# Kernel optimization log

Measured on AMD Instinct MI355X. Metric: run time of the kernel, lower is better.

The kernel has to match this reference:

```python
import jax, jax.numpy as jnp
import numpy as np

D_MODEL = 1024
H = 16
D_K = D_MODEL // H
NEG = -1e9


def setup_inputs() -> dict:
    key = jax.random.key(0)
    ks = jax.random.split(key, 13)
    B, S = 4, 2048
    q = jax.random.normal(ks[0], (B, S, D_MODEL), dtype=jnp.float32)
    k = jax.random.normal(ks[1], (B, S, D_MODEL), dtype=jnp.float32)
    v = jax.random.normal(ks[2], (B, S, D_MODEL), dtype=jnp.float32)
    mask = jax.random.randint(ks[3], (B, 1, S, S), 0, 2, dtype=jnp.int32)
    s = 1.0 / np.sqrt(D_MODEL)
    wq = jax.random.uniform(ks[4], (D_MODEL, D_MODEL), jnp.float32, -s, s)
    bq = jax.random.uniform(ks[5], (D_MODEL,), jnp.float32, -s, s)
    wk = jax.random.uniform(ks[6], (D_MODEL, D_MODEL), jnp.float32, -s, s)
    bk = jax.random.uniform(ks[7], (D_MODEL,), jnp.float32, -s, s)
    wv = jax.random.uniform(ks[8], (D_MODEL, D_MODEL), jnp.float32, -s, s)
    bv = jax.random.uniform(ks[9], (D_MODEL,), jnp.float32, -s, s)
    wo = jax.random.uniform(ks[10], (D_MODEL, D_MODEL), jnp.float32, -s, s)
    bo = jax.random.uniform(ks[11], (D_MODEL,), jnp.float32, -s, s)
    return {"q": q, "k": k, "v": v, "mask": mask,
            "wq": wq, "bq": bq, "wk": wk, "bk": bk,
            "wv": wv, "bv": bv, "wo": wo, "bo": bo}


def reference(q, k, v, mask, wq, bq, wk, bk, wv, bv, wo, bo):
    B, S, _ = q.shape
    # projections (torch Linear: x @ W.T + b)
    query = q @ wq.T + bq
    key_ = k @ wk.T + bk
    value = v @ wv.T + bv
    # [B, S, H, D_K] -> [B, H, S, D_K]
    query = query.reshape(B, S, H, D_K).transpose(0, 2, 1, 3)
    key_ = key_.reshape(B, S, H, D_K).transpose(0, 2, 1, 3)
    value = value.reshape(B, S, H, D_K).transpose(0, 2, 1, 3)
    scores = jnp.einsum('bhqd,bhkd->bhqk', query, key_) / jnp.sqrt(jnp.float32(D_K))
    scores = jnp.where(mask == 0, jnp.float32(NEG), scores)
    attn = jax.nn.softmax(scores, axis=-1)  # dropout p=0 -> identity
    x = jnp.einsum('bhqk,bhkd->bhqd', attn, value)
    x = x.transpose(0, 2, 1, 3).reshape(B, S, D_MODEL)
    return x @ wo.T + bo
```

## Files before the change

### kernel.cpp

```cpp
#include <hip/hip_runtime.h>
#include <stdint.h>
#include <stddef.h>


typedef unsigned short ushort_t;
typedef unsigned long long u64;
typedef __attribute__((ext_vector_type(8))) short short8;
typedef __attribute__((ext_vector_type(4))) float floatx4;
typedef __attribute__((ext_vector_type(4))) unsigned short ushort4v;
typedef __attribute__((ext_vector_type(4))) unsigned int uint4v;

#define QSCALE (0.125f * 1.4426950408889634f)

__device__ __forceinline__ ushort_t f2bf(float f) {
    union { float ff; unsigned int i; } v; v.ff = f;
    unsigned int u = v.i;
    return (ushort_t)((u + 0x7fffu + ((u >> 16) & 1u)) >> 16);
}
__device__ __forceinline__ unsigned int pack2bf(float a, float b) {
    union { float f; unsigned int i; } ua, ub; ua.f = a; ub.f = b;
    return ((ua.i + 0x8000u) >> 16) | ((ub.i + 0x8000u) & 0xffff0000u);
}
__device__ __forceinline__ float fexp2(float x) {
#if __has_builtin(__builtin_amdgcn_exp2f)
    return __builtin_amdgcn_exp2f(x);
#else
    return exp2f(x);
#endif
}
__device__ __forceinline__ void g2l16(const void* g, void* l) {
    __builtin_amdgcn_global_load_lds(
        (const __attribute__((address_space(1))) void*)(uintptr_t)g,
        (__attribute__((address_space(3))) void*)(uint32_t)(uintptr_t)l,
        16, 0, 0);
}

__global__ __launch_bounds__(256) void conv_w4(
    const float* __restrict__ w0, const float* __restrict__ w1,
    const float* __restrict__ w2, const float* __restrict__ w3,
    ushort_t* __restrict__ out)
{
    const int seg = blockIdx.y;
    const float* src = (seg == 0) ? w0 : (seg == 1) ? w1 : (seg == 2) ? w2 : w3;
    const int i = blockIdx.x * 256 + threadIdx.x;
    const float4 v = ((const float4*)src)[i];
    ushort4v o;
    o.x = f2bf(v.x); o.y = f2bf(v.y); o.z = f2bf(v.z); o.w = f2bf(v.w);
    ((ushort4v*)(out + (size_t)seg * 1024 * 1024))[i] = o;
}

__global__ __launch_bounds__(256) void mask_pack(
    const int* __restrict__ m, u64* __restrict__ out)
{
    const int gid = blockIdx.x * 256 + threadIdx.x;
    const u64 bits = __ballot(m[gid] != 0);
    if ((threadIdx.x & 63) == 0) out[gid >> 6] = bits;
}

template <int MODE, int AF32>
__global__ __launch_bounds__(256, 2) void gemm_bt(
    const void* __restrict__ Ain, const ushort_t* __restrict__ W,
    const float* __restrict__ bias, void* __restrict__ Cout, float scale)
{
    constexpr int N = 1024, K = 1024;
    __shared__ alignas(16) ushort_t As[128 * 32];
    __shared__ alignas(16) ushort_t Bs[128 * 32];

    const int tid  = threadIdx.x;
    const int lane = tid & 63;
    const int w    = tid >> 6;
    const int quad = lane >> 4;
    const int l16  = lane & 15;
    const int wm = w >> 1, wn = w & 1;
    const int bm = blockIdx.x * 128, bn = blockIdx.y * 128;

    const int ar0 = tid >> 2,         acs0 = ((tid & 3) ^ (ar0 & 3)) * 8;
    const int ar1 = (tid + 256) >> 2, acs1 = ((tid & 3) ^ (ar1 & 3)) * 8;

    const ushort_t* Wst0 = W + (size_t)(bn + ar0) * K + acs0;
    const ushort_t* Wst1 = W + (size_t)(bn + ar1) * K + acs1;

    const int arow = tid >> 1, ahalf = tid & 1;
    const float* Af = (const float*)Ain + (size_t)(bm + arow) * K + ahalf * 16;
    const int ac0 = ((2 * ahalf + 0) ^ (arow & 3)) * 8;
    const int ac1 = ((2 * ahalf + 1) ^ (arow & 3)) * 8;

    const ushort_t* Ast0 = (const ushort_t*)Ain + (size_t)(bm + ar0) * K + acs0;
    const ushort_t* Ast1 = (const ushort_t*)Ain + (size_t)(bm + ar1) * K + acs1;

    const int ksw = (quad ^ (l16 & 3)) * 8;
    int asoff[4], bsoff[4];
#pragma unroll
    for (int i = 0; i < 4; i++) {
        asoff[i] = (wm * 64 + i * 16 + l16) * 32 + ksw;
        bsoff[i] = (wn * 64 + i * 16 + l16) * 32 + ksw;
    }

    floatx4 acc[4][4] = {};

    for (int kt = 0; kt < K; kt += 32) {
        float4 f0, f1, f2, f3;
        if (AF32) {
            const float4* ap = (const float4*)(Af + kt);
            f0 = ap[0]; f1 = ap[1]; f2 = ap[2]; f3 = ap[3];
        }
        __syncthreads();
        if (AF32) {
            uint4v c0, c1;
            c0.x = pack2bf(f0.x, f0.y); c0.y = pack2bf(f0.z, f0.w);
            c0.z = pack2bf(f1.x, f1.y); c0.w = pack2bf(f1.z, f1.w);
            c1.x = pack2bf(f2.x, f2.y); c1.y = pack2bf(f2.z, f2.w);
            c1.z = pack2bf(f3.x, f3.y); c1.w = pack2bf(f3.z, f3.w);
            *(uint4v*)&As[arow * 32 + ac0] = c0;
            *(uint4v*)&As[arow * 32 + ac1] = c1;
        } else {
            g2l16(Ast0 + kt, &As[tid * 8]);
            g2l16(Ast1 + kt, &As[(tid + 256) * 8]);
        }
        g2l16(Wst0 + kt, &Bs[tid * 8]);
        g2l16(Wst1 + kt, &Bs[(tid + 256) * 8]);
        __syncthreads();

        short8 af[4], bf[4];
#pragma unroll
        for (int i = 0; i < 4; i++) af[i] = *(const short8*)&As[asoff[i]];
#pragma unroll
        for (int i = 0; i < 4; i++) bf[i] = *(const short8*)&Bs[bsoff[i]];
#pragma unroll
        for (int mi = 0; mi < 4; mi++)
#pragma unroll
            for (int ni = 0; ni < 4; ni++)
                acc[mi][ni] = __builtin_amdgcn_mfma_f32_16x16x32_bf16(
                    af[mi], bf[ni], acc[mi][ni], 0, 0, 0);
    }

#pragma unroll
    for (int ni = 0; ni < 4; ni++) {
        const int n = bn + wn * 64 + ni * 16 + l16;
        const float bv = bias[n];
#pragma unroll
        for (int mi = 0; mi < 4; mi++) {
            const int mbase = bm + wm * 64 + mi * 16 + quad * 4;
            if (MODE == 2) {
                const int b_ = mbase >> 11, s0 = mbase & 2047;
                const int h = n >> 6, d = n & 63;
                ushort4v pk;
#pragma unroll
                for (int r = 0; r < 4; r++)
                    pk[r] = f2bf((acc[mi][ni][r] + bv) * scale);
                *(ushort4v*)&((ushort_t*)Cout)[
                    (((size_t)(b_ * 16 + h)) * 64 + d) * 2048 + s0] = pk;
            } else {
#pragma unroll
                for (int r = 0; r < 4; r++) {
                    const int m = mbase + r;
                    const float of = (acc[mi][ni][r] + bv) * scale;
                    if (MODE == 0) {
                        ((float*)Cout)[(size_t)m * N + n] = of;
                    } else {
                        const int b_ = m >> 11, s = m & 2047;
                        const int h = n >> 6, d = n & 63;
                        ((ushort_t*)Cout)[(((size_t)(b_ * 16 + h)) * 2048 + s) * 64 + d]
                            = f2bf(of);
                    }
                }
            }
        }
    }
}

__global__ __launch_bounds__(256, 3) void attn(
    const ushort_t* __restrict__ Q,
    const ushort_t* __restrict__ Kk,
    const ushort_t* __restrict__ Vt,
    const u64* __restrict__ mb,
    ushort_t* __restrict__ X)
{
    constexpr int S = 2048;
    __shared__ alignas(16) ushort_t Ks[64 * 64];
    __shared__ alignas(16) ushort_t Vs[64 * 64];
    __shared__ alignas(16) ushort_t Ps[4][16 * 64];

    const int tid  = threadIdx.x;
    const int lane = tid & 63;
    const int w    = tid >> 6;
    const int quad = lane >> 4;
    const int l16  = lane & 15;
    const int bh = blockIdx.x;
    const int b  = bh >> 4, h = bh & 15;
    const int qbase = blockIdx.y * 64 + w * 16;
    const int qlane = qbase + l16;

    const int r0 = tid >> 3,         cs0 = ((tid & 7) ^ (r0 & 7)) * 8;
    const int r1 = (tid + 256) >> 3, cs1 = ((tid & 7) ^ (r1 & 7)) * 8;

    const ushort_t* Kst0 = &Kk[((size_t)bh * S + r0) * 64 + cs0];
    const ushort_t* Kst1 = &Kk[((size_t)bh * S + r1) * 64 + cs1];
    const ushort_t* Vst0 = &Vt[((size_t)bh * 64 + r0) * S + cs0];
    const ushort_t* Vst1 = &Vt[((size_t)bh * 64 + r1) * S + cs1];

    const int swz = l16 & 7;
    int kvoff[2][4], pfoff[2], pwoff[4];
#pragma unroll
    for (int ks = 0; ks < 2; ks++) {
        pfoff[ks] = l16 * 64 + (((ks * 4 + quad) ^ swz) * 8);
#pragma unroll
        for (int ni = 0; ni < 4; ni++)
            kvoff[ks][ni] = (ni * 16 + l16) * 64 + (((ks * 4 + quad) ^ swz) * 8);
    }
#pragma unroll
    for (int ni = 0; ni < 4; ni++)
        pwoff[ni] = l16 * 64 + (((ni * 2 + (quad >> 1)) ^ swz) * 8) + (quad & 1) * 4;
    ushort_t* Psw = &Ps[w][0];

    short8 qf[2];
#pragma unroll
    for (int ks = 0; ks < 2; ks++)
        qf[ks] = *(const short8*)&Q[((size_t)bh * S + qlane) * 64 + ks * 32 + quad * 8];

    short8 onesv;
#pragma unroll
    for (int i = 0; i < 8; i++) onesv[i] = (short)0x3F80;

    const u64* mrow = mb + ((size_t)b * S + qlane) * 32;

    floatx4 o[4] = {};
    floatx4 lf = {};

    for (int kt = 0; kt < 32; kt++) {
        __syncthreads();
        g2l16(Kst0 + kt * 4096, &Ks[tid * 8]);
        g2l16(Kst1 + kt * 4096, &Ks[(tid + 256) * 8]);
        g2l16(Vst0 + kt * 64,   &Vs[tid * 8]);
        g2l16(Vst1 + kt * 64,   &Vs[(tid + 256) * 8]);
        __syncthreads();

        floatx4 s[4] = {};
#pragma unroll
        for (int ks = 0; ks < 2; ks++)
#pragma unroll
            for (int ni = 0; ni < 4; ni++)
                s[ni] = __builtin_amdgcn_mfma_f32_16x16x32_bf16(
                    *(const short8*)&Ks[kvoff[ks][ni]], qf[ks], s[ni], 0, 0, 0);

        const u64 mw = mrow[kt];
#pragma unroll
        for (int ni = 0; ni < 4; ni++) {
            const unsigned int t = (unsigned int)(mw >> (ni * 16 + quad * 4));
#pragma unroll
            for (int r = 0; r < 4; r++)
                s[ni][r] = (t & (1u << r)) ? fexp2(s[ni][r]) : 0.f;
        }

#pragma unroll
        for (int ni = 0; ni < 4; ni++) {
            unsigned int lo = pack2bf(s[ni][0], s[ni][1]);
            unsigned int hi = pack2bf(s[ni][2], s[ni][3]);
            unsigned long long dv = ((unsigned long long)hi << 32) | lo;
            *(unsigned long long*)&Psw[pwoff[ni]] = dv;
        }

#pragma unroll
        for (int ks = 0; ks < 2; ks++) {
            const short8 pf = *(const short8*)&Psw[pfoff[ks]];
            lf = __builtin_amdgcn_mfma_f32_16x16x32_bf16(onesv, pf, lf, 0, 0, 0);
#pragma unroll
            for (int ni = 0; ni < 4; ni++)
                o[ni] = __builtin_amdgcn_mfma_f32_16x16x32_bf16(
                    *(const short8*)&Vs[kvoff[ks][ni]], pf, o[ni], 0, 0, 0);
        }
    }

    const float inv = 1.0f / lf[0];
#pragma unroll
    for (int ni = 0; ni < 4; ni++) {
        ushort4v pk;
#pragma unroll
        for (int r = 0; r < 4; r++) pk[r] = f2bf(o[ni][r] * inv);
        *(ushort4v*)&X[((size_t)b * S + qlane) * 1024 + h * 64 + ni * 16 + quad * 4] = pk;
    }
}

extern "C" void kernel_launch(void* const* d_in, const int* in_sizes, int n_in,
                              void* d_out, int out_size, void* d_ws, size_t ws_size,
                              hipStream_t stream) {
    const float* q    = (const float*)d_in[0];
    const float* k    = (const float*)d_in[1];
    const float* v    = (const float*)d_in[2];
    const int*   mask = (const int*)d_in[3];
    const float* wq   = (const float*)d_in[4];
    const float* bq   = (const float*)d_in[5];
    const float* wk   = (const float*)d_in[6];
    const float* bk   = (const float*)d_in[7];
    const float* wv   = (const float*)d_in[8];
    const float* bv   = (const float*)d_in[9];
    const float* wo   = (const float*)d_in[10];
    const float* bo   = (const float*)d_in[11];

    const size_t MB = 1024 * 1024;
    uint8_t* ws = (uint8_t*)d_ws;
    ushort_t* Wb   = (ushort_t*)(ws);
    u64*      mbits= (u64*)(ws + 8 * MB);
    ushort_t* Qp   = (ushort_t*)(ws + 10 * MB);
    ushort_t* Kp   = (ushort_t*)(ws + 26 * MB);
    ushort_t* Vtp  = (ushort_t*)(ws + 42 * MB);
    ushort_t* Xp   = (ushort_t*)(ws + 58 * MB);

    dim3 blk(256);
    dim3 gg(64, 8);
    const int gW = (1024 * 1024) / 1024;
    const int gM = (4 * 2048 * 2048) / 256;

    conv_w4<<<dim3(gW, 4), blk, 0, stream>>>(wq, wk, wv, wo, Wb);
    mask_pack<<<gM, blk, 0, stream>>>(mask, mbits);

    gemm_bt<1, 1><<<gg, blk, 0, stream>>>(q, Wb,                bq, Qp,  QSCALE);
    gemm_bt<1, 1><<<gg, blk, 0, stream>>>(k, Wb + 1 * MB,       bk, Kp,  1.0f);
    gemm_bt<2, 1><<<gg, blk, 0, stream>>>(v, Wb + 2 * MB,       bv, Vtp, 1.0f);

    attn<<<dim3(64, 32), blk, 0, stream>>>(Qp, Kp, Vtp, mbits, Xp);

    gemm_bt<0, 0><<<gg, blk, 0, stream>>>(Xp, Wb + 3 * MB,      bo, d_out, 1.0f);
}
```

Before: 475.0 us.

## Batch QKV GEMMs into one launch, prefetch A, and double attention key tile

Merges the three QKV projection launches into a single gemm_qkv kernel indexed by blockIdx.z, and swaps the grid axes so consecutive blocks share the same activation rows. The fp32 A tile is now loaded one iteration ahead to hide global latency behind the MFMA work, and occupancy is raised to 3 blocks. The attention kernel processes 128 keys per iteration instead of 64, halving barrier and loop overhead at the cost of double the LDS per block, which may lower occupancy. The output GEMM becomes a separate specialised bf16 kernel.

New measurement: 483.0 us. About the same (+1.7%).

```diff
diff --git a/kernel.cpp b/kernel.cpp
--- a/kernel.cpp
+++ b/kernel.cpp
@@ -57,14 +57,23 @@
     if ((threadIdx.x & 63) == 0) out[gid >> 6] = bits;
 }
 
-template <int MODE, int AF32>
-__global__ __launch_bounds__(256, 2) void gemm_bt(
-    const void* __restrict__ Ain, const ushort_t* __restrict__ W,
-    const float* __restrict__ bias, void* __restrict__ Cout, float scale)
+__global__ __launch_bounds__(256, 3) void gemm_qkv(
+    const float* __restrict__ qin, const float* __restrict__ kin,
+    const float* __restrict__ vin, const ushort_t* __restrict__ Wall,
+    const float* __restrict__ bqp, const float* __restrict__ bkp,
+    const float* __restrict__ bvp, ushort_t* __restrict__ Qp,
+    ushort_t* __restrict__ Kp, ushort_t* __restrict__ Vtp)
 {
-    constexpr int N = 1024, K = 1024;
+    constexpr int K = 1024;
     __shared__ alignas(16) ushort_t As[128 * 32];
     __shared__ alignas(16) ushort_t Bs[128 * 32];
+
+    const int z = blockIdx.z;
+    const float* Ain = (z == 0) ? qin : (z == 1) ? kin : vin;
+    const ushort_t* W = Wall + (size_t)z * 1024 * 1024;
+    const float* bias = (z == 0) ? bqp : (z == 1) ? bkp : bvp;
+    const float scale = (z == 0) ? QSCALE : 1.0f;
+    ushort_t* Cout = (z == 0) ? Qp : (z == 1) ? Kp : Vtp;
 
     const int tid  = threadIdx.x;
     const int lane = tid & 63;
@@ -72,21 +81,17 @@
     const int quad = lane >> 4;
     const int l16  = lane & 15;
     const int wm = w >> 1, wn = w & 1;
-    const int bm = blockIdx.x * 128, bn = blockIdx.y * 128;
+    const int bm = blockIdx.y * 128, bn = blockIdx.x * 128;
 
     const int ar0 = tid >> 2,         acs0 = ((tid & 3) ^ (ar0 & 3)) * 8;
     const int ar1 = (tid + 256) >> 2, acs1 = ((tid & 3) ^ (ar1 & 3)) * 8;
-
     const ushort_t* Wst0 = W + (size_t)(bn + ar0) * K + acs0;
     const ushort_t* Wst1 = W + (size_t)(bn + ar1) * K + acs1;
 
     const int arow = tid >> 1, ahalf = tid & 1;
-    const float* Af = (const float*)Ain + (size_t)(bm + arow) * K + ahalf * 16;
+    const float* Af = Ain + (size_t)(bm + arow) * K + ahalf * 16;
     const int ac0 = ((2 * ahalf + 0) ^ (arow & 3)) * 8;
     const int ac1 = ((2 * ahalf + 1) ^ (arow & 3)) * 8;
-
-    const ushort_t* Ast0 = (const ushort_t*)Ain + (size_t)(bm + ar0) * K + acs0;
-    const ushort_t* Ast1 = (const ushort_t*)Ain + (size_t)(bm + ar1) * K + acs1;
 
     const int ksw = (quad ^ (l16 & 3)) * 8;
     int asoff[4], bsoff[4];
@@ -98,28 +103,31 @@
 
     floatx4 acc[4][4] = {};
 
+    float4 fA0, fA1, fA2, fA3;
+    {
+        const float4* ap = (const float4*)Af;
+        fA0 = ap[0]; fA1 = ap[1]; fA2 = ap[2]; fA3 = ap[3];
+    }
+
     for (int kt = 0; kt < K; kt += 32) {
-        float4 f0, f1, f2, f3;
-        if (AF32) {
-            const float4* ap = (const float4*)(Af + kt);
-            f0 = ap[0]; f1 = ap[1]; f2 = ap[2]; f3 = ap[3];
-        }
-        __syncthreads();
-        if (AF32) {
+        __syncthreads();
+        {
             uint4v c0, c1;
-            c0.x = pack2bf(f0.x, f0.y); c0.y = pack2bf(f0.z, f0.w);
-            c0.z = pack2bf(f1.x, f1.y); c0.w = pack2bf(f1.z, f1.w);
-            c1.x = pack2bf(f2.x, f2.y); c1.y = pack2bf(f2.z, f2.w);
-            c1.z = pack2bf(f3.x, f3.y); c1.w = pack2bf(f3.z, f3.w);
+            c0.x = pack2bf(fA0.x, fA0.y); c0.y = pack2bf(fA0.z, fA0.w);
+            c0.z = pack2bf(fA1.x, fA1.y); c0.w = pack2bf(fA1.z, fA1.w);
+            c1.x = pack2bf(fA2.x, fA2.y); c1.y = pack2bf(fA2.z, fA2.w);
+            c1.z = pack2bf(fA3.x, fA3.y); c1.w = pack2bf(fA3.z, fA3.w);
             *(uint4v*)&As[arow * 32 + ac0] = c0;
             *(uint4v*)&As[arow * 32 + ac1] = c1;
-        } else {
-            g2l16(Ast0 + kt, &As[tid * 8]);
-            g2l16(Ast1 + kt, &As[(tid + 256) * 8]);
         }
         g2l16(Wst0 + kt, &Bs[tid * 8]);
         g2l16(Wst1 + kt, &Bs[(tid + 256) * 8]);
         __syncthreads();
+
+        if (kt + 32 < K) {
+            const float4* ap = (const float4*)(Af + kt + 32);
+            fA0 = ap[0]; fA1 = ap[1]; fA2 = ap[2]; fA3 = ap[3];
+        }
 
         short8 af[4], bf[4];
 #pragma unroll
@@ -138,33 +146,95 @@
     for (int ni = 0; ni < 4; ni++) {
         const int n = bn + wn * 64 + ni * 16 + l16;
         const float bv = bias[n];
+        const int h = n >> 6, d = n & 63;
 #pragma unroll
         for (int mi = 0; mi < 4; mi++) {
             const int mbase = bm + wm * 64 + mi * 16 + quad * 4;
-            if (MODE == 2) {
-                const int b_ = mbase >> 11, s0 = mbase & 2047;
-                const int h = n >> 6, d = n & 63;
+            const int b_ = mbase >> 11;
+            if (z == 2) {
+                const int s0 = mbase & 2047;
                 ushort4v pk;
 #pragma unroll
                 for (int r = 0; r < 4; r++)
-                    pk[r] = f2bf((acc[mi][ni][r] + bv) * scale);
-                *(ushort4v*)&((ushort_t*)Cout)[
-                    (((size_t)(b_ * 16 + h)) * 64 + d) * 2048 + s0] = pk;
+                    pk[r] = f2bf(acc[mi][ni][r] + bv);
+                *(ushort4v*)&Cout[(((size_t)(b_ * 16 + h)) * 64 + d) * 2048 + s0] = pk;
             } else {
 #pragma unroll
                 for (int r = 0; r < 4; r++) {
-                    const int m = mbase + r;
-                    const float of = (acc[mi][ni][r] + bv) * scale;
-                    if (MODE == 0) {
-                        ((float*)Cout)[(size_t)m * N + n] = of;
-                    } else {
-                        const int b_ = m >> 11, s = m & 2047;
-                        const int h = n >> 6, d = n & 63;
-                        ((ushort_t*)Cout)[(((size_t)(b_ * 16 + h)) * 2048 + s) * 64 + d]
-                            = f2bf(of);
-                    }
+                    const int s = (mbase + r) & 2047;
+                    Cout[(((size_t)(b_ * 16 + h)) * 2048 + s) * 64 + d]
+                        = f2bf((acc[mi][ni][r] + bv) * scale);
                 }
             }
+        }
+    }
+}
+
+__global__ __launch_bounds__(256, 2) void gemm_out(
+    const ushort_t* __restrict__ A, const ushort_t* __restrict__ W,
+    const float* __restrict__ bias, float* __restrict__ Cout)
+{
+    constexpr int N = 1024, K = 1024;
+    __shared__ alignas(16) ushort_t As[128 * 32];
+    __shared__ alignas(16) ushort_t Bs[128 * 32];
+
+    const int tid  = threadIdx.x;
+    const int lane = tid & 63;
+    const int w    = tid >> 6;
+    const int quad = lane >> 4;
+    const int l16  = lane & 15;
+    const int wm = w >> 1, wn = w & 1;
+    const int bm = blockIdx.y * 128, bn = blockIdx.x * 128;
+
+    const int ar0 = tid >> 2,         acs0 = ((tid & 3) ^ (ar0 & 3)) * 8;
+    const int ar1 = (tid + 256) >> 2, acs1 = ((tid & 3) ^ (ar1 & 3)) * 8;
+
+    const ushort_t* Ast0 = A + (size_t)(bm + ar0) * K + acs0;
+    const ushort_t* Ast1 = A + (size_t)(bm + ar1) * K + acs1;
+    const ushort_t* Wst0 = W + (size_t)(bn + ar0) * K + acs0;
+    const ushort_t* Wst1 = W + (size_t)(bn + ar1) * K + acs1;
+
+    const int ksw = (quad ^ (l16 & 3)) * 8;
+    int asoff[4], bsoff[4];
+#pragma unroll
+    for (int i = 0; i < 4; i++) {
+        asoff[i] = (wm * 64 + i * 16 + l16) * 32 + ksw;
+        bsoff[i] = (wn * 64 + i * 16 + l16) * 32 + ksw;
+    }
+
+    floatx4 acc[4][4] = {};
+
+    for (int kt = 0; kt < K; kt += 32) {
+        __syncthreads();
+        g2l16(Ast0 + kt, &As[tid * 8]);
+        g2l16(Ast1 + kt, &As[(tid + 256) * 8]);
+        g2l16(Wst0 + kt, &Bs[tid * 8]);
+        g2l16(Wst1 + kt, &Bs[(tid + 256) * 8]);
+        __syncthreads();
+
+        short8 af[4], bf[4];
+#pragma unroll
+        for (int i = 0; i < 4; i++) af[i] = *(const short8*)&As[asoff[i]];
+#pragma unroll
+        for (int i = 0; i < 4; i++) bf[i] = *(const short8*)&Bs[bsoff[i]];
+#pragma unroll
+        for (int mi = 0; mi < 4; mi++)
+#pragma unroll
+            for (int ni = 0; ni < 4; ni++)
+                acc[mi][ni] = __builtin_amdgcn_mfma_f32_16x16x32_bf16(
+                    af[mi], bf[ni], acc[mi][ni], 0, 0, 0);
+    }
+
+#pragma unroll
+    for (int ni = 0; ni < 4; ni++) {
+        const int n = bn + wn * 64 + ni * 16 + l16;
+        const float bv = bias[n];
+#pragma unroll
+        for (int mi = 0; mi < 4; mi++) {
+            const int mbase = bm + wm * 64 + mi * 16 + quad * 4;
+#pragma unroll
+            for (int r = 0; r < 4; r++)
+                Cout[(size_t)(mbase + r) * N + n] = acc[mi][ni][r] + bv;
         }
     }
 }
@@ -177,9 +247,9 @@
     ushort_t* __restrict__ X)
 {
     constexpr int S = 2048;
-    __shared__ alignas(16) ushort_t Ks[64 * 64];
-    __shared__ alignas(16) ushort_t Vs[64 * 64];
-    __shared__ alignas(16) ushort_t Ps[4][16 * 64];
+    __shared__ alignas(16) ushort_t Ks[128 * 64];
+    __shared__ alignas(16) ushort_t Vs[64 * 128];
+    __shared__ alignas(16) ushort_t Ps[4][16 * 128];
 
     const int tid  = threadIdx.x;
     const int lane = tid & 63;
@@ -188,29 +258,39 @@
     const int l16  = lane & 15;
     const int bh = blockIdx.x;
     const int b  = bh >> 4, h = bh & 15;
-    const int qbase = blockIdx.y * 64 + w * 16;
-    const int qlane = qbase + l16;
-
-    const int r0 = tid >> 3,         cs0 = ((tid & 7) ^ (r0 & 7)) * 8;
-    const int r1 = (tid + 256) >> 3, cs1 = ((tid & 7) ^ (r1 & 7)) * 8;
-
-    const ushort_t* Kst0 = &Kk[((size_t)bh * S + r0) * 64 + cs0];
-    const ushort_t* Kst1 = &Kk[((size_t)bh * S + r1) * 64 + cs1];
-    const ushort_t* Vst0 = &Vt[((size_t)bh * 64 + r0) * S + cs0];
-    const ushort_t* Vst1 = &Vt[((size_t)bh * 64 + r1) * S + cs1];
+    const int qlane = blockIdx.y * 64 + w * 16 + l16;
+
+    const ushort_t* Kst[4];
+    const ushort_t* Vst[4];
+#pragma unroll
+    for (int p = 0; p < 4; p++) {
+        const int idx = tid + 256 * p;
+        const int kr = idx >> 3, kc = (idx & 7) ^ (kr & 7);
+        Kst[p] = &Kk[((size_t)bh * S + kr) * 64 + kc * 8];
+        const int vr = idx >> 4, vpos = idx & 15;
+        const int vc = (vpos & 8) | ((vpos & 7) ^ (vr & 7));
+        Vst[p] = &Vt[((size_t)bh * 64 + vr) * S + vc * 8];
+    }
 
     const int swz = l16 & 7;
-    int kvoff[2][4], pfoff[2], pwoff[4];
-#pragma unroll
-    for (int ks = 0; ks < 2; ks++) {
-        pfoff[ks] = l16 * 64 + (((ks * 4 + quad) ^ swz) * 8);
-#pragma unroll
-        for (int ni = 0; ni < 4; ni++)
-            kvoff[ks][ni] = (ni * 16 + l16) * 64 + (((ks * 4 + quad) ^ swz) * 8);
-    }
-#pragma unroll
-    for (int ni = 0; ni < 4; ni++)
-        pwoff[ni] = l16 * 64 + (((ni * 2 + (quad >> 1)) ^ swz) * 8) + (quad & 1) * 4;
+    int kbase[2];
+#pragma unroll
+    for (int ks = 0; ks < 2; ks++)
+        kbase[ks] = l16 * 64 + (((ks * 4 + quad) ^ swz) * 8);
+    int vbase[4];
+#pragma unroll
+    for (int ks = 0; ks < 4; ks++) {
+        const int c = ks * 4 + quad;
+        const int pos = (c & 8) | ((c & 7) ^ swz);
+        vbase[ks] = l16 * 128 + pos * 8;
+    }
+    int pwoff[8];
+#pragma unroll
+    for (int ni = 0; ni < 8; ni++) {
+        const int c = ni * 2 + (quad >> 1);
+        const int pos = (c & 8) | ((c & 7) ^ swz);
+        pwoff[ni] = l16 * 128 + pos * 8 + (quad & 1) * 4;
+    }
     ushort_t* Psw = &Ps[w][0];
 
     short8 qf[2];
@@ -227,47 +307,49 @@
     floatx4 o[4] = {};
     floatx4 lf = {};
 
-    for (int kt = 0; kt < 32; kt++) {
-        __syncthreads();
-        g2l16(Kst0 + kt * 4096, &Ks[tid * 8]);
-        g2l16(Kst1 + kt * 4096, &Ks[(tid + 256) * 8]);
-        g2l16(Vst0 + kt * 64,   &Vs[tid * 8]);
-        g2l16(Vst1 + kt * 64,   &Vs[(tid + 256) * 8]);
-        __syncthreads();
-
-        floatx4 s[4] = {};
+    for (int kt = 0; kt < 16; kt++) {
+        __syncthreads();
+#pragma unroll
+        for (int p = 0; p < 4; p++) {
+            g2l16(Kst[p] + kt * 8192, &Ks[(tid + 256 * p) * 8]);
+            g2l16(Vst[p] + kt * 128,  &Vs[(tid + 256 * p) * 8]);
+        }
+        __syncthreads();
+
+        floatx4 s[8] = {};
 #pragma unroll
         for (int ks = 0; ks < 2; ks++)
 #pragma unroll
-            for (int ni = 0; ni < 4; ni++)
+            for (int ni = 0; ni < 8; ni++)
                 s[ni] = __builtin_amdgcn_mfma_f32_16x16x32_bf16(
-                    *(const short8*)&Ks[kvoff[ks][ni]], qf[ks], s[ni], 0, 0, 0);
-
-        const u64 mw = mrow[kt];
-#pragma unroll
-        for (int ni = 0; ni < 4; ni++) {
-            const unsigned int t = (unsigned int)(mw >> (ni * 16 + quad * 4));
+                    *(const short8*)&Ks[kbase[ks] + ni * 1024], qf[ks], s[ni], 0, 0, 0);
+
+        const u64 w0 = mrow[2 * kt], w1 = mrow[2 * kt + 1];
+#pragma unroll
+        for (int ni = 0; ni < 8; ni++) {
+            const unsigned int t =
+                (unsigned int)(((ni < 4) ? w0 : w1) >> ((ni & 3) * 16 + quad * 4));
 #pragma unroll
             for (int r = 0; r < 4; r++)
                 s[ni][r] = (t & (1u << r)) ? fexp2(s[ni][r]) : 0.f;
         }
 
 #pragma unroll
-        for (int ni = 0; ni < 4; ni++) {
-            unsigned int lo = pack2bf(s[ni][0], s[ni][1]);
-            unsigned int hi = pack2bf(s[ni][2], s[ni][3]);
-            unsigned long long dv = ((unsigned long long)hi << 32) | lo;
-            *(unsigned long long*)&Psw[pwoff[ni]] = dv;
-        }
-
-#pragma unroll
-        for (int ks = 0; ks < 2; ks++) {
-            const short8 pf = *(const short8*)&Psw[pfoff[ks]];
+        for (int ni = 0; ni < 8; ni++) {
+            const unsigned int lo = pack2bf(s[ni][0], s[ni][1]);
+            const unsigned int hi = pack2bf(s[ni][2], s[ni][3]);
+            *(unsigned long long*)&Psw[pwoff[ni]] =
+                ((unsigned long long)hi << 32) | lo;
+        }
+
+#pragma unroll
+        for (int ks = 0; ks < 4; ks++) {
+            const short8 pf = *(const short8*)&Psw[vbase[ks]];
             lf = __builtin_amdgcn_mfma_f32_16x16x32_bf16(onesv, pf, lf, 0, 0, 0);
 #pragma unroll
             for (int ni = 0; ni < 4; ni++)
                 o[ni] = __builtin_amdgcn_mfma_f32_16x16x32_bf16(
-                    *(const short8*)&Vs[kvoff[ks][ni]], pf, o[ni], 0, 0, 0);
+                    *(const short8*)&Vs[vbase[ks] + ni * 2048], pf, o[ni], 0, 0, 0);
         }
     }
 
@@ -307,18 +389,16 @@
     ushort_t* Xp   = (ushort_t*)(ws + 58 * MB);
 
     dim3 blk(256);
-    dim3 gg(64, 8);
     const int gW = (1024 * 1024) / 1024;
     const int gM = (4 * 2048 * 2048) / 256;
 
     conv_w4<<<dim3(gW, 4), blk, 0, stream>>>(wq, wk, wv, wo, Wb);
     mask_pack<<<gM, blk, 0, stream>>>(mask, mbits);
 
-    gemm_bt<1, 1><<<gg, blk, 0, stream>>>(q, Wb,                bq, Qp,  QSCALE);
-    gemm_bt<1, 1><<<gg, blk, 0, stream>>>(k, Wb + 1 * MB,       bk, Kp,  1.0f);
-    gemm_bt<2, 1><<<gg, blk, 0, stream>>>(v, Wb + 2 * MB,       bv, Vtp, 1.0f);
+    gemm_qkv<<<dim3(8, 64, 3), blk, 0, stream>>>(
+        q, k, v, Wb, bq, bk, bv, Qp, Kp, Vtp);
 
     attn<<<dim3(64, 32), blk, 0, stream>>>(Qp, Kp, Vtp, mbits, Xp);
 
-    gemm_bt<0, 0><<<gg, blk, 0, stream>>>(Xp, Wb + 3 * MB,      bo, d_out, 1.0f);
-}
+    gemm_out<<<dim3(8, 64), blk, 0, stream>>>(Xp, Wb + 3 * MB, bo, (float*)d_out);
+}
```
